# Optimization experiments

Measured on AMD Instinct MI355X. Metric: run time of the kernel, lower is better.

## Reference

```python
import jax, jax.numpy as jnp
import numpy as np

B, T_ENC, T_DEC = 32, 512, 32
ENC = DEC = EMB = ATT = OUT = 256
VOCAB = 32000
CHUNK = 8
SOS = 1


def _energy(enc, h, W, V, b, vv, g, vb, r):
    # enc: [B,T,ENC], h: [B,DEC] -> [B,T]
    t = jnp.tanh(enc @ W.T + (h @ V.T)[:, None, :] + b)           # [B,T,ATT]
    w_eff = (g[0] / jnp.linalg.norm(vv)) * vv                      # weight-normed v
    return t @ w_eff + vb[0] + r[0]


def _excl_cumprod(x):
    # exclusive safe cumprod along axis 1: [1, x0, x0*x1, ...]
    logs = jnp.cumsum(jnp.log(jnp.clip(x, 1e-10, 1.0)), axis=1)
    logs = jnp.concatenate([jnp.zeros_like(logs[:, :1]), logs[:, :-1]], axis=1)
    return jnp.exp(logs)


def _moving_sum(x, back, forward):
    # sliding-window sum over axis 1, window [j-back, j+forward]
    T = x.shape[1]
    w = back + forward + 1
    xp = jnp.pad(x, ((0, 0), (back, forward)))
    c = jnp.cumsum(xp, axis=1)
    c = jnp.concatenate([jnp.zeros_like(c[:, :1]), c], axis=1)
    return c[:, w:w + T] - c[:, :T]


def _chunkwise_beta(alpha, u, w):
    u = u - jnp.max(u, axis=1, keepdims=True)
    eu = jnp.exp(u)
    denom = jnp.clip(_moving_sum(eu, w - 1, 0), 1e-10, None)
    return eu * _moving_sum(alpha / denom, 0, w - 1)


def setup_inputs():
    key = jax.random.key(0)
    ks = jax.random.split(key, 20)
    s = 0.05
    rn = lambda k, shp: jax.random.normal(k, shp, jnp.float32) * s
    return {
        'encoder_outputs': jax.random.normal(ks[0], (B, T_ENC, ENC), jnp.float32),
        'decoder_inputs': jax.random.randint(ks[1], (B, T_DEC), 0, VOCAB),
        'h0': jax.random.normal(ks[2], (B, DEC), jnp.float32),
        'noise': jax.random.normal(ks[3], (T_DEC, B, T_ENC), jnp.float32),
        'emb': rn(ks[4], (VOCAB, EMB)),
        'W_ih': rn(ks[5], (DEC, EMB)), 'b_ih': jnp.zeros((DEC,), jnp.float32),
        'W_hh': rn(ks[6], (DEC, DEC)), 'b_hh': jnp.zeros((DEC,), jnp.float32),
        'Wm': rn(ks[7], (ATT, ENC)), 'Vm': rn(ks[8], (ATT, DEC)),
        'bm': rn(ks[9], (ATT,)), 'vvm': jax.random.normal(ks[10], (ATT,), jnp.float32),
        'gm': jnp.full((1,), (1.0 / ATT) ** 0.5, jnp.float32),
        'vbm': jnp.zeros((1,), jnp.float32), 'rm': jnp.full((1,), -4.0, jnp.float32),
        'Wc': rn(ks[11], (ATT, ENC)), 'Vc': rn(ks[12], (ATT, DEC)),
        'bc': rn(ks[13], (ATT,)), 'vvc': jax.random.normal(ks[14], (ATT,), jnp.float32),
        'gc': jnp.full((1,), (1.0 / ATT) ** 0.5, jnp.float32),
        'vbc': jnp.zeros((1,), jnp.float32), 'rc': jnp.full((1,), -4.0, jnp.float32),
        'W_comb': rn(ks[15], (OUT, ENC + DEC)),
        'W_proj': rn(ks[16], (VOCAB, OUT)), 'b_proj': jnp.zeros((VOCAB,), jnp.float32),
    }


def reference(encoder_outputs, decoder_inputs, h0, noise, emb,
              W_ih, b_ih, W_hh, b_hh,
              Wm, Vm, bm, vvm, gm, vbm, rm,
              Wc, Vc, bc, vvc, gc, vbc, rc,
              W_comb, W_proj, b_proj):
    batch = encoder_outputs.shape[0]
    alpha0 = jnp.zeros((batch, encoder_outputs.shape[1]), encoder_outputs.dtype).at[:, 0].set(1.0)
    x0 = jnp.full((batch,), SOS, dtype=decoder_inputs.dtype)

    def step(carry, xs):
        x_tok, h, alpha = carry
        noise_t, next_tok = xs
        x = emb[x_tok]                                             # embedding lookup
        h = jnp.tanh(x @ W_ih.T + b_ih + h @ W_hh.T + b_hh)        # RNNCell (tanh)
        e_m = _energy(encoder_outputs, h, Wm, Vm, bm, vvm, gm, vbm, rm)
        p = jax.nn.sigmoid(e_m + noise_t)
        cp = _excl_cumprod(1.0 - p)
        alpha = p * cp * jnp.cumsum(alpha / jnp.clip(cp, 1e-10, 1.0), axis=1)
        e_c = _energy(encoder_outputs, h, Wc, Vc, bc, vvc, gc, vbc, rc)
        beta = _chunkwise_beta(alpha, e_c, CHUNK)
        context = jnp.einsum('bt,bte->be', beta, encoder_outputs)
        attn = jnp.tanh(jnp.concatenate([context, h], axis=1) @ W_comb.T)
        logit = attn @ W_proj.T + b_proj
        return (next_tok, h, alpha), logit

    xs = (noise, decoder_inputs.T)
    _, logits = jax.lax.scan(step, (x0, h0, alpha0), xs)           # [T_dec,B,V]
    return jnp.transpose(logits, (1, 0, 2))                        # [B,T_dec,V]
```

## Files before the change

kernel.cpp:

```cpp
#include <hip/hip_runtime.h>
#include <cstddef>

#define B 32
#define T_ENC 512
#define T_DEC 32
#define E 256
#define VOCAB 32000
#define SOS 1

typedef __attribute__((ext_vector_type(8))) short short8;
typedef __attribute__((ext_vector_type(4))) float floatx4;

static const size_t OFF_ENCW   = 0;
static const size_t OFF_WEFFM  = OFF_ENCW + (size_t)B * T_ENC * 2 * E;
static const size_t OFF_WEFFC  = OFF_WEFFM + E;
static const size_t OFF_BSUM   = OFF_WEFFC + E;
static const size_t OFF_XIH    = OFF_BSUM + E;
static const size_t OFF_WHHT   = OFF_XIH + (size_t)T_DEC * B * E;
static const size_t OFF_VMT    = OFF_WHHT + (size_t)E * E;
static const size_t OFF_VCT    = OFF_VMT + (size_t)E * E;
static const size_t OFF_WCOMBT = OFF_VCT + (size_t)E * E;
static const size_t OFF_ATTNB  = OFF_WCOMBT + (size_t)2 * E * E;
static const size_t OFF_WPBF   = OFF_ATTNB + (size_t)T_DEC * B * E / 2;

static const size_t OUT_EMBX  = 0;
static const size_t OUT_BETA  = 262144;
static const size_t OUT_ACOMB = 786432;
static const size_t OUT_HALL  = 1310720;
static const size_t OUT_HV    = 1572864;
static const size_t OUT_PE    = 2097152;
static const size_t OUT_VMC   = 3145728;
static const size_t OUT_ZERO  = 3276800;
static const size_t OUT_WHI   = 3277312;
static const size_t OUT_WLO   = 3342848;
static const size_t OUT_B512  = 3408384;

__device__ __forceinline__ float ftanh(float x) {
  float ax = __builtin_fabsf(x);
  float e  = __expf(-2.f * ax);
  float r  = (1.f - e) * __builtin_amdgcn_rcpf(1.f + e);
  return __builtin_copysignf(r, x);
}

__device__ __forceinline__ float fsigmoid(float z) {
  return __builtin_amdgcn_rcpf(1.f + __expf(-z));
}

__device__ __forceinline__ float wredsum(float s) {
  s += __shfl_xor(s, 1, 64);  s += __shfl_xor(s, 2, 64);  s += __shfl_xor(s, 4, 64);
  s += __shfl_xor(s, 8, 64);  s += __shfl_xor(s, 16, 64); s += __shfl_xor(s, 32, 64);
  return s;
}

__device__ __forceinline__ float wredmax(float s) {
  s = fmaxf(s, __shfl_xor(s, 1, 64));  s = fmaxf(s, __shfl_xor(s, 2, 64));
  s = fmaxf(s, __shfl_xor(s, 4, 64));  s = fmaxf(s, __shfl_xor(s, 8, 64));
  s = fmaxf(s, __shfl_xor(s, 16, 64)); s = fmaxf(s, __shfl_xor(s, 32, 64));
  return s;
}

__device__ __forceinline__ unsigned short f2bf(float f) {
  unsigned int u = __float_as_uint(f);
  u = (u + 0x7fffu + ((u >> 16) & 1u)) >> 16;
  return (unsigned short)u;
}

__device__ __forceinline__ float bf2f(unsigned short h) {
  return __uint_as_float((unsigned int)h << 16);
}

__device__ __forceinline__ float wexcl(float tot, int lane) {
  float v = tot;
#pragma unroll
  for (int off = 1; off < 64; off <<= 1) {
    float y = __shfl_up(v, off, 64);
    if (lane >= off) v += y;
  }
  return v - tot;
}

__global__ __launch_bounds__(256) void prep_misc(
    const float* __restrict__ vvm, const float* __restrict__ gm, float* __restrict__ w_effm,
    const float* __restrict__ vvc, const float* __restrict__ gc, float* __restrict__ w_effc,
    const float* __restrict__ b_ih, const float* __restrict__ b_hh, float* __restrict__ bsum,
    const float* __restrict__ bm, const float* __restrict__ bc, float* __restrict__ bias512,
    const float* __restrict__ Vm, const float* __restrict__ Vc,
    float* __restrict__ Vmc, float* __restrict__ zero512,
    const float* __restrict__ Wm, const float* __restrict__ Wc,
    unsigned short* __restrict__ Whi, unsigned short* __restrict__ Wlo)
{
  __shared__ float red[256];
  const int blk = blockIdx.x, tid = threadIdx.x;
  if (blk < 2) {
    const float* vv = blk ? vvc : vvm;
    const float* g  = blk ? gc  : gm;
    float* out      = blk ? w_effc : w_effm;
    float v = vv[tid];
    red[tid] = v * v;
    __syncthreads();
    for (int off = 128; off > 0; off >>= 1) {
      if (tid < off) red[tid] += red[tid + off];
      __syncthreads();
    }
    float norm = sqrtf(red[0]);
    out[tid] = (g[0] / norm) * v;
  } else if (blk == 2) {
    bsum[tid] = b_ih[tid] + b_hh[tid];
    bias512[tid]       = bm[tid];
    bias512[256 + tid] = bc[tid];
    zero512[tid] = 0.f;
    zero512[256 + tid] = 0.f;
  } else if (blk < 131) {
    int i = (blk - 3) * 1024 + tid * 4;
    float4 v = (i < E * E) ? *(const float4*)(Vm + i) : *(const float4*)(Vc + i - E * E);
    *(float4*)(Vmc + i) = v;
  } else {
    int i = (blk - 131) * 1024 + tid * 4;
    float4 v = (i < E * E) ? *(const float4*)(Wm + i) : *(const float4*)(Wc + i - E * E);
    ushort4 h, l;
    h.x = f2bf(v.x); l.x = f2bf(v.x - bf2f(h.x));
    h.y = f2bf(v.y); l.y = f2bf(v.y - bf2f(h.y));
    h.z = f2bf(v.z); l.z = f2bf(v.z - bf2f(h.z));
    h.w = f2bf(v.w); l.w = f2bf(v.w - bf2f(h.w));
    *(ushort4*)(Whi + i) = h;
    *(ushort4*)(Wlo + i) = l;
  }
}

__global__ __launch_bounds__(256) void transpose2(
    const float* __restrict__ W_hh, float* __restrict__ W_hhT,
    const float* __restrict__ W_comb, float* __restrict__ W_combT)
{
  __shared__ float tl[32][33];
  const int blk = blockIdx.x;
  const float* in; float* out; int C, bx, by;
  if (blk < 64) { in = W_hh;   out = W_hhT;   C = 256; bx = blk & 7;  by = blk >> 3; }
  else { int k = blk - 64; in = W_comb; out = W_combT; C = 512; bx = k & 15; by = k >> 4; }
  const int R = 256;
  const int tx = threadIdx.x & 31, ty = threadIdx.x >> 5;
  const int c0 = bx * 32, r0 = by * 32;
#pragma unroll
  for (int k = 0; k < 4; k++)
    tl[ty + 8 * k][tx] = in[(size_t)(r0 + ty + 8 * k) * C + c0 + tx];
  __syncthreads();
#pragma unroll
  for (int k = 0; k < 4; k++)
    out[(size_t)(c0 + ty + 8 * k) * R + r0 + tx] = tl[tx][ty + 8 * k];
}

__global__ __launch_bounds__(256) void gather_emb(
    const int* __restrict__ dec, const float* __restrict__ emb, float* __restrict__ embX)
{
  int r = blockIdx.x, d = threadIdx.x;
  int s = r >> 5, b = r & 31;
  int tok = (s == 0) ? SOS : dec[b * T_DEC + s - 1];
  embX[(size_t)r * E + d] = emb[(size_t)tok * E + d];
}

__global__ __launch_bounds__(256) void cvt_bf16(
    const float* __restrict__ src, unsigned short* __restrict__ dst)
{
  size_t i = ((size_t)blockIdx.x * 256 + threadIdx.x) * 4;
  float4 v = *(const float4*)(src + i);
  ushort4 o;
  o.x = f2bf(v.x); o.y = f2bf(v.y); o.z = f2bf(v.z); o.w = f2bf(v.w);
  *(ushort4*)(dst + i) = o;
}

__global__ __launch_bounds__(256) void gemm_xwt(
    const float* __restrict__ A, const float* __restrict__ W,
    const float* __restrict__ bias, float* __restrict__ Y,
    int M, int N, int K)
{
  __shared__ float As[64][68];
  __shared__ float Ws[64][68];
  const int tid = threadIdx.x;
  const int tx = tid & 15, ty = tid >> 4;
  const int row0 = blockIdx.y * 64, col0 = blockIdx.x * 64;
  float acc[4][4];
#pragma unroll
  for (int i = 0; i < 4; i++)
#pragma unroll
    for (int j = 0; j < 4; j++) acc[i][j] = 0.f;

  for (int k0 = 0; k0 < K; k0 += 64) {
#pragma unroll
    for (int s = 0; s < 4; s++) {
      int i = (s << 4) + ty;
      int j = tx << 2;
      float4 av = *(const float4*)(A + (size_t)(row0 + i) * K + k0 + j);
      As[j][i] = av.x; As[j + 1][i] = av.y; As[j + 2][i] = av.z; As[j + 3][i] = av.w;
      float4 wv = *(const float4*)(W + (size_t)(col0 + i) * K + k0 + j);
      Ws[j][i] = wv.x; Ws[j + 1][i] = wv.y; Ws[j + 2][i] = wv.z; Ws[j + 3][i] = wv.w;
    }
    __syncthreads();
#pragma unroll
    for (int kk = 0; kk < 64; kk++) {
      const float4 af = *(const float4*)&As[kk][ty << 2];
      const float4 bf = *(const float4*)&Ws[kk][tx << 2];
      acc[0][0] += af.x * bf.x; acc[0][1] += af.x * bf.y; acc[0][2] += af.x * bf.z; acc[0][3] += af.x * bf.w;
      acc[1][0] += af.y * bf.x; acc[1][1] += af.y * bf.y; acc[1][2] += af.y * bf.z; acc[1][3] += af.y * bf.w;
      acc[2][0] += af.z * bf.x; acc[2][1] += af.z * bf.y; acc[2][2] += af.z * bf.z; acc[2][3] += af.z * bf.w;
      acc[3][0] += af.w * bf.x; acc[3][1] += af.w * bf.y; acc[3][2] += af.w * bf.z; acc[3][3] += af.w * bf.w;
    }
    __syncthreads();
  }
  const float4 bv = *(const float4*)(bias + col0 + (tx << 2));
#pragma unroll
  for (int i = 0; i < 4; i++) {
    float4 o;
    o.x = acc[i][0] + bv.x; o.y = acc[i][1] + bv.y;
    o.z = acc[i][2] + bv.z; o.w = acc[i][3] + bv.w;
    *(float4*)(Y + (size_t)(row0 + (ty << 2) + i) * N + col0 + (tx << 2)) = o;
  }
}

__global__ __launch_bounds__(256) void enc_mfma(
    const float* __restrict__ A,
    const unsigned short* __restrict__ Whi, const unsigned short* __restrict__ Wlo,
    const float* __restrict__ bias512, float* __restrict__ Y)
{
  __shared__ unsigned short a_hi[64][264];
  __shared__ unsigned short a_lo[64][264];
  const int tid = threadIdx.x;
  const int row0 = blockIdx.x * 64;
#pragma unroll
  for (int u = 0; u < 16; ++u) {
    int f = tid + (u << 8);
    int r = f >> 6, c = (f & 63) << 2;
    float4 v = *(const float4*)(A + (size_t)(row0 + r) * E + c);
    ushort4 h, l;
    h.x = f2bf(v.x); l.x = f2bf(v.x - bf2f(h.x));
    h.y = f2bf(v.y); l.y = f2bf(v.y - bf2f(h.y));
    h.z = f2bf(v.z); l.z = f2bf(v.z - bf2f(h.z));
    h.w = f2bf(v.w); l.w = f2bf(v.w - bf2f(h.w));
    *(ushort4*)&a_hi[r][c] = h;
    *(ushort4*)&a_lo[r][c] = l;
  }
  __syncthreads();
  const int lane = tid & 63, w = tid >> 6;
  const int m = lane & 15, q = lane >> 4;
  const int colbase = w << 7;
#pragma unroll
  for (int cp = 0; cp < 4; ++cp) {
    const int c0 = colbase + (cp << 5);
    floatx4 acc[4][2] = {};
    for (int k0 = 0; k0 < E; k0 += 32) {
      const size_t w0 = (size_t)(c0 + m) * E + (q << 3) + k0;
      const size_t w1 = (size_t)(c0 + 16 + m) * E + (q << 3) + k0;
      short8 bh0 = *(const short8*)(Whi + w0);
      short8 bl0 = *(const short8*)(Wlo + w0);
      short8 bh1 = *(const short8*)(Whi + w1);
      short8 bl1 = *(const short8*)(Wlo + w1);
#pragma unroll
      for (int rg = 0; rg < 4; ++rg) {
        short8 ah = *(const short8*)&a_hi[(rg << 4) + m][(q << 3) + k0];
        short8 al = *(const short8*)&a_lo[(rg << 4) + m][(q << 3) + k0];
        acc[rg][0] = __builtin_amdgcn_mfma_f32_16x16x32_bf16(ah, bh0, acc[rg][0], 0, 0, 0);
        acc[rg][0] = __builtin_amdgcn_mfma_f32_16x16x32_bf16(al, bh0, acc[rg][0], 0, 0, 0);
        acc[rg][0] = __builtin_amdgcn_mfma_f32_16x16x32_bf16(ah, bl0, acc[rg][0], 0, 0, 0);
        acc[rg][0] = __builtin_amdgcn_mfma_f32_16x16x32_bf16(al, bl0, acc[rg][0], 0, 0, 0);
        acc[rg][1] = __builtin_amdgcn_mfma_f32_16x16x32_bf16(ah, bh1, acc[rg][1], 0, 0, 0);
        acc[rg][1] = __builtin_amdgcn_mfma_f32_16x16x32_bf16(al, bh1, acc[rg][1], 0, 0, 0);
        acc[rg][1] = __builtin_amdgcn_mfma_f32_16x16x32_bf16(ah, bl1, acc[rg][1], 0, 0, 0);
        acc[rg][1] = __builtin_amdgcn_mfma_f32_16x16x32_bf16(al, bl1, acc[rg][1], 0, 0, 0);
      }
    }
    const float bia0 = bias512[c0 + m], bia1 = bias512[c0 + 16 + m];
#pragma unroll
    for (int rg = 0; rg < 4; ++rg)
#pragma unroll
      for (int r = 0; r < 4; ++r) {
        const size_t row = row0 + (rg << 4) + (q << 2) + r;
        Y[row * (2 * E) + c0 + m]      = acc[rg][0][r] + bia0;
        Y[row * (2 * E) + c0 + 16 + m] = acc[rg][1][r] + bia1;
      }
  }
}

__global__ __launch_bounds__(1024) void hchain_kernel(
    const float* __restrict__ Xih, const float* __restrict__ W_hhT,
    const float* __restrict__ h0,
    float* __restrict__ A_comb, float* __restrict__ h_all)
{
  __shared__ float h_s[E];
  __shared__ float red[1024];
  const int b = blockIdx.x, tid = threadIdx.x;
  const int c = tid >> 8, d = tid & 255, k0 = c * 64;
  float wreg[64];
#pragma unroll
  for (int j = 0; j < 64; ++j) wreg[j] = W_hhT[(size_t)(k0 + j) * E + d];
  if (tid < E) h_s[tid] = h0[(size_t)b * E + tid];
  __syncthreads();
  for (int s = 0; s < T_DEC; ++s) {
    float acc = 0.f;
#pragma unroll
    for (int j = 0; j < 64; j += 4) {
      float4 hh = *(const float4*)&h_s[k0 + j];
      acc += hh.x * wreg[j] + hh.y * wreg[j + 1] + hh.z * wreg[j + 2] + hh.w * wreg[j + 3];
    }
    red[tid] = acc;
    __syncthreads();
    if (tid < E) {
      float v = red[tid] + red[256 + tid] + red[512 + tid] + red[768 + tid]
              + Xih[((size_t)s * B + b) * E + tid];
      float hh = ftanh(v);
      h_s[tid] = hh;
      A_comb[((size_t)(b * T_DEC + s)) * (2 * E) + E + tid] = hh;
      h_all[((size_t)(b * T_DEC + s)) * E + tid] = hh;
    }
    __syncthreads();
  }
}

__global__ __launch_bounds__(256) void energy_kernel(
    const float* __restrict__ encW, const float* __restrict__ g_hv,
    const float* __restrict__ w_effm, const float* __restrict__ w_effc,
    const float* __restrict__ vbm, const float* __restrict__ rmp,
    const float* __restrict__ vbc, const float* __restrict__ rcp_,
    float* __restrict__ g_pe)
{
  __shared__ float hvm[T_DEC * E];
  __shared__ float hvc[T_DEC * E];
  const int b = blockIdx.x, t0 = blockIdx.y << 4;
  const int tid = threadIdx.x, lane = tid & 63, w = tid >> 6;
  const float* hvb = g_hv + ((size_t)b * T_DEC) * (2 * E);
  for (int i = tid * 4; i < T_DEC * 2 * E; i += 1024) {
    float4 v = *(const float4*)(hvb + i);
    int s = i >> 9, dd = i & 511;
    if (dd < E) *(float4*)&hvm[s * E + dd]     = v;
    else        *(float4*)&hvc[s * E + dd - E] = v;
  }
  __syncthreads();
  const float embias = vbm[0] + rmp[0];
  const float ecbias = vbc[0] + rcp_[0];
  const float4 wm4 = *(const float4*)(w_effm + lane * 4);
  const float4 wc4 = *(const float4*)(w_effc + lane * 4);
  const int t = t0 + (w << 2);
  const size_t rb = ((size_t)(b * T_ENC + t)) * (2 * E) + lane * 4;
  const float4 em0 = *(const float4*)(encW + rb);
  const float4 em1 = *(const float4*)(encW + rb + 512);
  const float4 em2 = *(const float4*)(encW + rb + 1024);
  const float4 em3 = *(const float4*)(encW + rb + 1536);
  const float4 ec0 = *(const float4*)(encW + rb + 256);
  const float4 ec1 = *(const float4*)(encW + rb + 768);
  const float4 ec2 = *(const float4*)(encW + rb + 1280);
  const float4 ec3 = *(const float4*)(encW + rb + 1792);
  float pv0 = 0.f, pv1 = 0.f, pv2 = 0.f, pv3 = 0.f;
  for (int s = 0; s < T_DEC; ++s) {
    const float4 hm4 = *(const float4*)&hvm[(s << 8) + lane * 4];
    const float4 hc4 = *(const float4*)&hvc[(s << 8) + lane * 4];
    float a0 = wm4.x * ftanh(em0.x + hm4.x) + wm4.y * ftanh(em0.y + hm4.y)
             + wm4.z * ftanh(em0.z + hm4.z) + wm4.w * ftanh(em0.w + hm4.w);
    float a1 = wm4.x * ftanh(em1.x + hm4.x) + wm4.y * ftanh(em1.y + hm4.y)
             + wm4.z * ftanh(em1.z + hm4.z) + wm4.w * ftanh(em1.w + hm4.w);
    float a2 = wm4.x * ftanh(em2.x + hm4.x) + wm4.y * ftanh(em2.y + hm4.y)
             + wm4.z * ftanh(em2.z + hm4.z) + wm4.w * ftanh(em2.w + hm4.w);
    float a3 = wm4.x * ftanh(em3.x + hm4.x) + wm4.y * ftanh(em3.y + hm4.y)
             + wm4.z * ftanh(em3.z + hm4.z) + wm4.w * ftanh(em3.w + hm4.w);
    float c0 = wc4.x * ftanh(ec0.x + hc4.x) + wc4.y * ftanh(ec0.y + hc4.y)
             + wc4.z * ftanh(ec0.z + hc4.z) + wc4.w * ftanh(ec0.w + hc4.w);
    float c1 = wc4.x * ftanh(ec1.x + hc4.x) + wc4.y * ftanh(ec1.y + hc4.y)
             + wc4.z * ftanh(ec1.z + hc4.z) + wc4.w * ftanh(ec1.w + hc4.w);
    float c2 = wc4.x * ftanh(ec2.x + hc4.x) + wc4.y * ftanh(ec2.y + hc4.y)
             + wc4.z * ftanh(ec2.z + hc4.z) + wc4.w * ftanh(ec2.w + hc4.w);
    float c3 = wc4.x * ftanh(ec3.x + hc4.x) + wc4.y * ftanh(ec3.y + hc4.y)
             + wc4.z * ftanh(ec3.z + hc4.z) + wc4.w * ftanh(ec3.w + hc4.w);
    a0 = wredsum(a0); a1 = wredsum(a1); a2 = wredsum(a2); a3 = wredsum(a3);
    c0 = wredsum(c0); c1 = wredsum(c1); c2 = wredsum(c2); c3 = wredsum(c3);
    if (lane == s) {
      pv0 = a0 + embias; pv1 = a1 + embias; pv2 = a2 + embias; pv3 = a3 + embias;
    }
    if (lane == 32 + s) {
      pv0 = c0 + ecbias; pv1 = c1 + ecbias; pv2 = c2 + ecbias; pv3 = c3 + ecbias;
    }
  }
  const size_t ob = (((size_t)b * T_ENC + t) << 6) + lane;
  g_pe[ob]       = pv0;
  g_pe[ob + 64]  = pv1;
  g_pe[ob + 128] = pv2;
  g_pe[ob + 192] = pv3;
}

__global__ __launch_bounds__(64) void scan_kernel(
    const float* __restrict__ g_pe, const float* __restrict__ noise,
    float* __restrict__ beta_all)
{
  const int b = blockIdx.x, lane = threadIdx.x;
  const float* pe = g_pe + ((size_t)b << 15);
  float alpha[8];
#pragma unroll
  for (int i = 0; i < 8; ++i) alpha[i] = 0.f;
  if (lane == 0) alpha[0] = 1.f;

  for (int s = 0; s < T_DEC; ++s) {
    const float* nrow = noise + ((size_t)s * B + b) * T_ENC + lane * 8;
    float4 n0 = *(const float4*)nrow;
    float4 n1 = *(const float4*)(nrow + 4);
    float nz[8] = {n0.x, n0.y, n0.z, n0.w, n1.x, n1.y, n1.z, n1.w};
    float p[8], ec[8];
#pragma unroll
    for (int i = 0; i < 8; ++i) {
      const size_t base = ((size_t)(lane * 8 + i)) << 6;
      float sm = pe[base + s];
      ec[i]    = pe[base + 32 + s];
      p[i] = fsigmoid(sm + nz[i]);
    }
    float lgv[8], lci[8], run = 0.f;
#pragma unroll
    for (int i = 0; i < 8; ++i) {
      float omp = fminf(fmaxf(1.f - p[i], 1e-10f), 1.f);
      lgv[i] = __logf(omp);
      run += lgv[i];
      lci[i] = run;
    }
    float ex1 = wexcl(run, lane);
    float cp[8], ao[8];
#pragma unroll
    for (int i = 0; i < 8; ++i) {
      float incl = lci[i] + ex1;
      cp[i] = __expf(incl - lgv[i]);
      float cpc = fminf(fmaxf(cp[i], 1e-10f), 1.f);
      ao[i] = alpha[i] * __builtin_amdgcn_rcpf(cpc);
    }
    float run2 = 0.f, lc2[8];
#pragma unroll
    for (int i = 0; i < 8; ++i) { run2 += ao[i]; lc2[i] = run2; }
    float ex2 = wexcl(run2, lane);
    float alpha_new[8];
#pragma unroll
    for (int i = 0; i < 8; ++i) alpha_new[i] = p[i] * cp[i] * (lc2[i] + ex2);
    float mloc = ec[0];
#pragma unroll
    for (int i = 1; i < 8; ++i) mloc = fmaxf(mloc, ec[i]);
    float mx = wredmax(mloc);
    float eu[8];
#pragma unroll
    for (int i = 0; i < 8; ++i) eu[i] = __expf(ec[i] - mx);
    float run3 = 0.f, c1[8];
#pragma unroll
    for (int i = 0; i < 8; ++i) { run3 += eu[i]; c1[i] = run3; }
    float ex3 = wexcl(run3, lane);
#pragma unroll
    for (int i = 0; i < 8; ++i) c1[i] += ex3;
    float r[8];
#pragma unroll
    for (int i = 0; i < 8; ++i) {
      float up = __shfl_up(c1[i], 1, 64);
      float prev = (lane == 0) ? 0.f : up;
      float denom = fmaxf(c1[i] - prev, 1e-10f);
      r[i] = alpha_new[i] * __builtin_amdgcn_rcpf(denom);
    }
    float run4 = 0.f, c2[8];
#pragma unroll
    for (int i = 0; i < 8; ++i) { run4 += r[i]; c2[i] = run4; }
    float ex4 = wexcl(run4, lane);
#pragma unroll
    for (int i = 0; i < 8; ++i) c2[i] += ex4;
    float c2_7 = c2[7];
    float dn[8];
#pragma unroll
    for (int i = 0; i < 8; ++i) dn[i] = __shfl_down(c2[i], 1, 64);
    float up7 = __shfl_up(c2_7, 1, 64);
    float beta[8];
#pragma unroll
    for (int i = 0; i < 8; ++i) {
      float hi = (i == 0) ? c2_7 : ((lane == 63) ? c2_7 : dn[i - 1]);
      float lo = (i == 0) ? ((lane == 0) ? 0.f : up7) : c2[i - 1];
      beta[i] = eu[i] * (hi - lo);
    }
    float* bp = beta_all + ((size_t)(b * T_DEC + s)) * T_ENC + lane * 8;
    *(float4*)bp       = (float4){beta[0], beta[1], beta[2], beta[3]};
    *(float4*)(bp + 4) = (float4){beta[4], beta[5], beta[6], beta[7]};
#pragma unroll
    for (int i = 0; i < 8; ++i) alpha[i] = alpha_new[i];
  }
}

__global__ __launch_bounds__(256) void context_kernel(
    const float* __restrict__ beta_all, const float* __restrict__ enc,
    float* __restrict__ A_comb)
{
  __shared__ float smem[T_ENC * 36];
  const int b = blockIdx.x, e0 = blockIdx.y << 6;
  const int tid = threadIdx.x;
  const float* bp = beta_all + (size_t)b * T_DEC * T_ENC;
  for (int i = tid; i < T_DEC * T_ENC; i += 256) {
    int s2 = i >> 9, t = i & 511;
    smem[t * 36 + s2] = bp[i];
  }
  __syncthreads();
  const int el = tid & 63, tg = tid >> 6;
  float4 a8[8];
#pragma unroll
  for (int u = 0; u < 8; ++u) a8[u] = (float4){0.f, 0.f, 0.f, 0.f};
  const float* ep = enc + (size_t)b * T_ENC * E + e0 + el;
  for (int t = tg; t < T_ENC; t += 4) {
    float v = ep[(size_t)t * E];
    const float4* bt = (const float4*)&smem[t * 36];
#pragma unroll
    for (int u = 0; u < 8; ++u) {
      float4 bv = bt[u];
      a8[u].x += bv.x * v; a8[u].y += bv.y * v;
      a8[u].z += bv.z * v; a8[u].w += bv.w * v;
    }
  }
  __syncthreads();
#pragma unroll
  for (int u = 0; u < 8; ++u) {
    smem[((tg * T_DEC + u * 4 + 0) << 6) + el] = a8[u].x;
    smem[((tg * T_DEC + u * 4 + 1) << 6) + el] = a8[u].y;
    smem[((tg * T_DEC + u * 4 + 2) << 6) + el] = a8[u].z;
    smem[((tg * T_DEC + u * 4 + 3) << 6) + el] = a8[u].w;
  }
  __syncthreads();
  for (int o = tid; o < T_DEC * 64; o += 256) {
    int s2 = o >> 6, e = o & 63;
    float v = smem[(s2 << 6) + e] + smem[((T_DEC + s2) << 6) + e]
            + smem[((2 * T_DEC + s2) << 6) + e] + smem[((3 * T_DEC + s2) << 6) + e];
    A_comb[((size_t)(b * T_DEC + s2)) * (2 * E) + e0 + e] = v;
  }
}

__global__ __launch_bounds__(256) void comb_tanh_kernel(
    const float* __restrict__ A, const float* __restrict__ Wt,
    unsigned short* __restrict__ attn_bf)
{
  __shared__ float As[64][68];
  __shared__ float Ws[64][68];
  const int tid = threadIdx.x, tx = tid & 15, ty = tid >> 4;
  const int row0 = blockIdx.y * 64, col0 = blockIdx.x * 64;
  float acc[4][4];
#pragma unroll
  for (int i = 0; i < 4; i++)
#pragma unroll
    for (int jj = 0; jj < 4; jj++) acc[i][jj] = 0.f;

  for (int k0 = 0; k0 < 2 * E; k0 += 64) {
#pragma unroll
    for (int ss = 0; ss < 4; ss++) {
      int i = (ss << 4) + ty;
      int jj = tx << 2;
      float4 av = *(const float4*)(A + (size_t)(row0 + i) * (2 * E) + k0 + jj);
      As[jj][i] = av.x; As[jj + 1][i] = av.y; As[jj + 2][i] = av.z; As[jj + 3][i] = av.w;
      float4 wv = *(const float4*)(Wt + (size_t)(k0 + i) * E + col0 + jj);
      *(float4*)&Ws[i][jj] = wv;
    }
    __syncthreads();
#pragma unroll
    for (int kk = 0; kk < 64; kk++) {
      const float4 af = *(const float4*)&As[kk][ty << 2];
      const float4 bf = *(const float4*)&Ws[kk][tx << 2];
      acc[0][0] += af.x * bf.x; acc[0][1] += af.x * bf.y; acc[0][2] += af.x * bf.z; acc[0][3] += af.x * bf.w;
      acc[1][0] += af.y * bf.x; acc[1][1] += af.y * bf.y; acc[1][2] += af.y * bf.z; acc[1][3] += af.y * bf.w;
      acc[2][0] += af.z * bf.x; acc[2][1] += af.z * bf.y; acc[2][2] += af.z * bf.z; acc[2][3] += af.z * bf.w;
      acc[3][0] += af.w * bf.x; acc[3][1] += af.w * bf.y; acc[3][2] += af.w * bf.z; acc[3][3] += af.w * bf.w;
    }
    __syncthreads();
  }
#pragma unroll
  for (int i = 0; i < 4; i++) {
    ushort4 o;
    o.x = f2bf(ftanh(acc[i][0])); o.y = f2bf(ftanh(acc[i][1]));
    o.z = f2bf(ftanh(acc[i][2])); o.w = f2bf(ftanh(acc[i][3]));
    *(ushort4*)(attn_bf + (size_t)(row0 + (ty << 2) + i) * E + col0 + (tx << 2)) = o;
  }
}

__global__ __launch_bounds__(256) void proj_mfma(
    const unsigned short* __restrict__ A, const unsigned short* __restrict__ Bw,
    const float* __restrict__ bias, float* __restrict__ Y)
{
  __shared__ unsigned short wl[64][264];
  __shared__ float tile[64][68];
  const int tid = threadIdx.x;
  const int wave = tid >> 6, lane = tid & 63;
  const int m = lane & 15, q = lane >> 4;
  const int col0 = blockIdx.x * 64;
#pragma unroll
  for (int u = 0; u < 16; ++u) {
    int f = tid + (u << 8);
    int r = f >> 6, c = (f & 63) << 2;
    *(ushort4*)&wl[r][c] = *(const ushort4*)(Bw + (size_t)(col0 + r) * E + c);
  }
  __syncthreads();

  for (int mt = 0; mt < 16; ++mt) {
    const int rowa = mt * 64 + wave * 16;
    floatx4 acc0 = {0.f, 0.f, 0.f, 0.f}, acc1 = acc0, acc2 = acc0, acc3 = acc0;
    const unsigned short* ar = A + (size_t)(rowa + m) * E + q * 8;
#pragma unroll
    for (int k0 = 0; k0 < E; k0 += 32) {
      short8 af = *(const short8*)(ar + k0);
      short8 b0 = *(const short8*)&wl[ 0 + m][q * 8 + k0];
      short8 b1 = *(const short8*)&wl[16 + m][q * 8 + k0];
      short8 b2 = *(const short8*)&wl[32 + m][q * 8 + k0];
      short8 b3 = *(const short8*)&wl[48 + m][q * 8 + k0];
      acc0 = __builtin_amdgcn_mfma_f32_16x16x32_bf16(af, b0, acc0, 0, 0, 0);
      acc1 = __builtin_amdgcn_mfma_f32_16x16x32_bf16(af, b1, acc1, 0, 0, 0);
      acc2 = __builtin_amdgcn_mfma_f32_16x16x32_bf16(af, b2, acc2, 0, 0, 0);
      acc3 = __builtin_amdgcn_mfma_f32_16x16x32_bf16(af, b3, acc3, 0, 0, 0);
    }
    const int rl = wave * 16 + q * 4;
#pragma unroll
    for (int r = 0; r < 4; r++) {
      tile[rl + r][ 0 + m] = acc0[r];
      tile[rl + r][16 + m] = acc1[r];
      tile[rl + r][32 + m] = acc2[r];
      tile[rl + r][48 + m] = acc3[r];
    }
    __syncthreads();
    const int row = tid >> 2, seg = tid & 3;
    const size_t yb = ((size_t)mt * 64 + row) * VOCAB + col0;
#pragma unroll
    for (int u = 0; u < 4; u++) {
      int cc = seg * 16 + u * 4;
      float4 v = *(const float4*)&tile[row][cc];
      float4 bb = *(const float4*)(bias + col0 + cc);
      v.x += bb.x; v.y += bb.y; v.z += bb.z; v.w += bb.w;
      *(float4*)(Y + yb + cc) = v;
    }
    __syncthreads();
  }
}

extern "C" void kernel_launch(void* const* d_in, const int* in_sizes, int n_in,
                              void* d_out, int out_size, void* d_ws, size_t ws_size,
                              hipStream_t stream)
{
  (void)in_sizes; (void)n_in; (void)out_size; (void)ws_size;
  const float* enc    = (const float*)d_in[0];
  const int*   dec    = (const int*)d_in[1];
  const float* h0     = (const float*)d_in[2];
  const float* noise  = (const float*)d_in[3];
  const float* emb    = (const float*)d_in[4];
  const float* W_ih   = (const float*)d_in[5];
  const float* b_ih   = (const float*)d_in[6];
  const float* W_hh   = (const float*)d_in[7];
  const float* b_hh   = (const float*)d_in[8];
  const float* Wm     = (const float*)d_in[9];
  const float* Vm     = (const float*)d_in[10];
  const float* bm     = (const float*)d_in[11];
  const float* vvm    = (const float*)d_in[12];
  const float* gm     = (const float*)d_in[13];
  const float* vbm    = (const float*)d_in[14];
  const float* rmp    = (const float*)d_in[15];
  const float* Wc     = (const float*)d_in[16];
  const float* Vc     = (const float*)d_in[17];
  const float* bc     = (const float*)d_in[18];
  const float* vvc    = (const float*)d_in[19];
  const float* gc     = (const float*)d_in[20];
  const float* vbc    = (const float*)d_in[21];
  const float* rcp_   = (const float*)d_in[22];
  const float* W_comb = (const float*)d_in[23];
  const float* W_proj = (const float*)d_in[24];
  const float* b_proj = (const float*)d_in[25];

  float* ws = (float*)d_ws;
  float* encW    = ws + OFF_ENCW;
  float* w_effm  = ws + OFF_WEFFM;
  float* w_effc  = ws + OFF_WEFFC;
  float* bsum    = ws + OFF_BSUM;
  float* Xih     = ws + OFF_XIH;
  float* W_hhT   = ws + OFF_WHHT;
  float* W_combT = ws + OFF_WCOMBT;
  unsigned short* attn_bf = (unsigned short*)(ws + OFF_ATTNB);
  unsigned short* Wp_bf   = (unsigned short*)(ws + OFF_WPBF);

  float* outF = (float*)d_out;
  float* embX     = outF + OUT_EMBX;
  float* beta_all = outF + OUT_BETA;
  float* A_comb   = outF + OUT_ACOMB;
  float* h_all    = outF + OUT_HALL;
  float* g_hv     = outF + OUT_HV;
  float* g_pe     = outF + OUT_PE;
  float* Vmc      = outF + OUT_VMC;
  float* zero512  = outF + OUT_ZERO;
  unsigned short* Whi = (unsigned short*)(outF + OUT_WHI);
  unsigned short* Wlo = (unsigned short*)(outF + OUT_WLO);
  float* bias512  = outF + OUT_B512;

  prep_misc<<<259, 256, 0, stream>>>(vvm, gm, w_effm, vvc, gc, w_effc,
                                     b_ih, b_hh, bsum, bm, bc, bias512,
                                     Vm, Vc, Vmc, zero512, Wm, Wc, Whi, Wlo);
  transpose2<<<192, 256, 0, stream>>>(W_hh, W_hhT, W_comb, W_combT);
  gather_emb<<<T_DEC * B, 256, 0, stream>>>(dec, emb, embX);
  gemm_xwt<<<dim3(E / 64, (T_DEC * B) / 64), 256, 0, stream>>>(embX, W_ih, bsum, Xih,
                                                               T_DEC * B, E, E);
  enc_mfma<<<(B * T_ENC) / 64, 256, 0, stream>>>(enc, Whi, Wlo, bias512, encW);
  cvt_bf16<<<(VOCAB * E) / 1024, 256, 0, stream>>>(W_proj, Wp_bf);

  hchain_kernel<<<B, 1024, 0, stream>>>(Xih, W_hhT, h0, A_comb, h_all);

  gemm_xwt<<<dim3((2 * E) / 64, (T_DEC * B) / 64), 256, 0, stream>>>(
      h_all, Vmc, zero512, g_hv, T_DEC * B, 2 * E, E);

  energy_kernel<<<dim3(B, T_ENC / 16), 256, 0, stream>>>(
      encW, g_hv, w_effm, w_effc, vbm, rmp, vbc, rcp_, g_pe);

  scan_kernel<<<B, 64, 0, stream>>>(g_pe, noise, beta_all);

  context_kernel<<<dim3(B, 4), 256, 0, stream>>>(beta_all, enc, A_comb);
  comb_tanh_kernel<<<dim3(E / 64, (T_DEC * B) / 64), 256, 0, stream>>>(A_comb, W_combT, attn_bf);
  proj_mfma<<<VOCAB / 64, 256, 0, stream>>>(attn_bf, Wp_bf, b_proj, outF);
}
```

Before: 633.9 us.

## Split energy kernel over decoder steps, use butterfly transpose-reduce, transpose pe layout

```diff
diff --git a/kernel.cpp b/kernel.cpp
--- a/kernel.cpp
+++ b/kernel.cpp
@@ -44,12 +44,6 @@
 
 __device__ __forceinline__ float fsigmoid(float z) {
   return __builtin_amdgcn_rcpf(1.f + __expf(-z));
-}
-
-__device__ __forceinline__ float wredsum(float s) {
-  s += __shfl_xor(s, 1, 64);  s += __shfl_xor(s, 2, 64);  s += __shfl_xor(s, 4, 64);
-  s += __shfl_xor(s, 8, 64);  s += __shfl_xor(s, 16, 64); s += __shfl_xor(s, 32, 64);
-  return s;
 }
 
 __device__ __forceinline__ float wredmax(float s) {
@@ -320,24 +314,21 @@
     const float* __restrict__ vbc, const float* __restrict__ rcp_,
     float* __restrict__ g_pe)
 {
-  __shared__ float hvm[T_DEC * E];
-  __shared__ float hvc[T_DEC * E];
-  const int b = blockIdx.x, t0 = blockIdx.y << 4;
+  __shared__ float hv_s[16 * 512];
+  const int b = blockIdx.x, t0 = blockIdx.y << 4, s0 = blockIdx.z << 4;
   const int tid = threadIdx.x, lane = tid & 63, w = tid >> 6;
-  const float* hvb = g_hv + ((size_t)b * T_DEC) * (2 * E);
-  for (int i = tid * 4; i < T_DEC * 2 * E; i += 1024) {
-    float4 v = *(const float4*)(hvb + i);
-    int s = i >> 9, dd = i & 511;
-    if (dd < E) *(float4*)&hvm[s * E + dd]     = v;
-    else        *(float4*)&hvc[s * E + dd - E] = v;
-  }
+  const float* hvb = g_hv + ((size_t)(b * T_DEC + s0)) * 512;
+  for (int i = tid * 4; i < 16 * 512; i += 1024)
+    *(float4*)&hv_s[i] = *(const float4*)(hvb + i);
   __syncthreads();
+
   const float embias = vbm[0] + rmp[0];
   const float ecbias = vbc[0] + rcp_[0];
+  const float bias_l = ((lane >> 2) & 1) ? ecbias : embias;
   const float4 wm4 = *(const float4*)(w_effm + lane * 4);
   const float4 wc4 = *(const float4*)(w_effc + lane * 4);
   const int t = t0 + (w << 2);
-  const size_t rb = ((size_t)(b * T_ENC + t)) * (2 * E) + lane * 4;
+  const size_t rb = ((size_t)(b * T_ENC + t)) * 512 + lane * 4;
   const float4 em0 = *(const float4*)(encW + rb);
   const float4 em1 = *(const float4*)(encW + rb + 512);
   const float4 em2 = *(const float4*)(encW + rb + 1024);
@@ -346,40 +337,50 @@
   const float4 ec1 = *(const float4*)(encW + rb + 768);
   const float4 ec2 = *(const float4*)(encW + rb + 1280);
   const float4 ec3 = *(const float4*)(encW + rb + 1792);
-  float pv0 = 0.f, pv1 = 0.f, pv2 = 0.f, pv3 = 0.f;
-  for (int s = 0; s < T_DEC; ++s) {
-    const float4 hm4 = *(const float4*)&hvm[(s << 8) + lane * 4];
-    const float4 hc4 = *(const float4*)&hvc[(s << 8) + lane * 4];
-    float a0 = wm4.x * ftanh(em0.x + hm4.x) + wm4.y * ftanh(em0.y + hm4.y)
+
+  const bool sb0 = lane & 1, sb1 = lane & 2, sb2 = lane & 4;
+  const int myr = lane >> 3;
+  float pv0 = 0.f, pv1 = 0.f;
+
+  for (int sl = 0; sl < 16; ++sl) {
+    const float4 hm4 = *(const float4*)&hv_s[(sl << 9) + lane * 4];
+    const float4 hc4 = *(const float4*)&hv_s[(sl << 9) + 256 + lane * 4];
+    float v0 = wm4.x * ftanh(em0.x + hm4.x) + wm4.y * ftanh(em0.y + hm4.y)
              + wm4.z * ftanh(em0.z + hm4.z) + wm4.w * ftanh(em0.w + hm4.w);
-    float a1 = wm4.x * ftanh(em1.x + hm4.x) + wm4.y * ftanh(em1.y + hm4.y)
+    float v1 = wm4.x * ftanh(em1.x + hm4.x) + wm4.y * ftanh(em1.y + hm4.y)
              + wm4.z * ftanh(em1.z + hm4.z) + wm4.w * ftanh(em1.w + hm4.w);
-    float a2 = wm4.x * ftanh(em2.x + hm4.x) + wm4.y * ftanh(em2.y + hm4.y)
+    float v2 = wm4.x * ftanh(em2.x + hm4.x) + wm4.y * ftanh(em2.y + hm4.y)
              + wm4.z * ftanh(em2.z + hm4.z) + wm4.w * ftanh(em2.w + hm4.w);
-    float a3 = wm4.x * ftanh(em3.x + hm4.x) + wm4.y * ftanh(em3.y + hm4.y)
+    float v3 = wm4.x * ftanh(em3.x + hm4.x) + wm4.y * ftanh(em3.y + hm4.y)
              + wm4.z * ftanh(em3.z + hm4.z) + wm4.w * ftanh(em3.w + hm4.w);
-    float c0 = wc4.x * ftanh(ec0.x + hc4.x) + wc4.y * ftanh(ec0.y + hc4.y)
+    float v4 = wc4.x * ftanh(ec0.x + hc4.x) + wc4.y * ftanh(ec0.y + hc4.y)
              + wc4.z * ftanh(ec0.z + hc4.z) + wc4.w * ftanh(ec0.w + hc4.w);
-    float c1 = wc4.x * ftanh(ec1.x + hc4.x) + wc4.y * ftanh(ec1.y + hc4.y)
+    float v5 = wc4.x * ftanh(ec1.x + hc4.x) + wc4.y * ftanh(ec1.y + hc4.y)
              + wc4.z * ftanh(ec1.z + hc4.z) + wc4.w * ftanh(ec1.w + hc4.w);
-    float c2 = wc4.x * ftanh(ec2.x + hc4.x) + wc4.y * ftanh(ec2.y + hc4.y)
+    float v6 = wc4.x * ftanh(ec2.x + hc4.x) + wc4.y * ftanh(ec2.y + hc4.y)
              + wc4.z * ftanh(ec2.z + hc4.z) + wc4.w * ftanh(ec2.w + hc4.w);
-    float c3 = wc4.x * ftanh(ec3.x + hc4.x) + wc4.y * ftanh(ec3.y + hc4.y)
+    float v7 = wc4.x * ftanh(ec3.x + hc4.x) + wc4.y * ftanh(ec3.y + hc4.y)
              + wc4.z * ftanh(ec3.z + hc4.z) + wc4.w * ftanh(ec3.w + hc4.w);
-    a0 = wredsum(a0); a1 = wredsum(a1); a2 = wredsum(a2); a3 = wredsum(a3);
-    c0 = wredsum(c0); c1 = wredsum(c1); c2 = wredsum(c2); c3 = wredsum(c3);
-    if (lane == s) {
-      pv0 = a0 + embias; pv1 = a1 + embias; pv2 = a2 + embias; pv3 = a3 + embias;
-    }
-    if (lane == 32 + s) {
-      pv0 = c0 + ecbias; pv1 = c1 + ecbias; pv2 = c2 + ecbias; pv3 = c3 + ecbias;
-    }
-  }
-  const size_t ob = (((size_t)b * T_ENC + t) << 6) + lane;
-  g_pe[ob]       = pv0;
-  g_pe[ob + 64]  = pv1;
-  g_pe[ob + 128] = pv2;
-  g_pe[ob + 192] = pv3;
+    float a0 = sb0 ? v1 : v0;  a0 += __shfl_xor(a0, 1, 64);
+    float a1 = sb0 ? v3 : v2;  a1 += __shfl_xor(a1, 1, 64);
+    float a2 = sb0 ? v5 : v4;  a2 += __shfl_xor(a2, 1, 64);
+    float a3 = sb0 ? v7 : v6;  a3 += __shfl_xor(a3, 1, 64);
+    float c0 = sb1 ? a1 : a0;  c0 += __shfl_xor(c0, 2, 64);
+    float c1 = sb1 ? a3 : a2;  c1 += __shfl_xor(c1, 2, 64);
+    float dd = sb2 ? c1 : c0;  dd += __shfl_xor(dd, 4, 64);
+    dd += __shfl_xor(dd, 8, 64);
+    dd += __shfl_xor(dd, 16, 64);
+    dd += __shfl_xor(dd, 32, 64);
+    float val = dd + bias_l;
+    if ((sl & 7) == myr) {
+      if (sl & 8) pv1 = val; else pv0 = val;
+    }
+  }
+  const int row_l = lane & 3, type = (lane >> 2) & 1;
+  const int tS = t0 + (w << 2) + row_l;
+  const int col = type * 32 + s0 + myr;
+  g_pe[((size_t)((b << 6) + col)) * 512 + tS]     = pv0;
+  g_pe[((size_t)((b << 6) + col + 8)) * 512 + tS] = pv1;
 }
 
 __global__ __launch_bounds__(64) void scan_kernel(
@@ -398,14 +399,17 @@
     float4 n0 = *(const float4*)nrow;
     float4 n1 = *(const float4*)(nrow + 4);
     float nz[8] = {n0.x, n0.y, n0.z, n0.w, n1.x, n1.y, n1.z, n1.w};
-    float p[8], ec[8];
-#pragma unroll
-    for (int i = 0; i < 8; ++i) {
-      const size_t base = ((size_t)(lane * 8 + i)) << 6;
-      float sm = pe[base + s];
-      ec[i]    = pe[base + 32 + s];
-      p[i] = fsigmoid(sm + nz[i]);
-    }
+    const float* psm = pe + (size_t)s * 512 + lane * 8;
+    const float* pec = pe + (size_t)(32 + s) * 512 + lane * 8;
+    float4 m0 = *(const float4*)psm;
+    float4 m1 = *(const float4*)(psm + 4);
+    float4 e0 = *(const float4*)pec;
+    float4 e1 = *(const float4*)(pec + 4);
+    float smv[8] = {m0.x, m0.y, m0.z, m0.w, m1.x, m1.y, m1.z, m1.w};
+    float ec[8]  = {e0.x, e0.y, e0.z, e0.w, e1.x, e1.y, e1.z, e1.w};
+    float p[8];
+#pragma unroll
+    for (int i = 0; i < 8; ++i) p[i] = fsigmoid(smv[i] + nz[i]);
     float lgv[8], lci[8], run = 0.f;
 #pragma unroll
     for (int i = 0; i < 8; ++i) {
@@ -695,7 +699,7 @@
   gemm_xwt<<<dim3((2 * E) / 64, (T_DEC * B) / 64), 256, 0, stream>>>(
       h_all, Vmc, zero512, g_hv, T_DEC * B, 2 * E, E);
 
-  energy_kernel<<<dim3(B, T_ENC / 16), 256, 0, stream>>>(
+  energy_kernel<<<dim3(B, T_ENC / 16, 2), 256, 0, stream>>>(
       encW, g_hv, w_effm, w_effc, vbm, rmp, vbc, rcp_, g_pe);
 
   scan_kernel<<<B, 64, 0, stream>>>(g_pe, noise, beta_all);
```

Measured after the change: 595.9 us. 6.0% less time.
